# Kernel optimization log

Measured on AMD Instinct MI355X. Metric: run time of the kernel, lower is better.

Reference implementation:

```python
import jax, jax.numpy as jnp
import numpy as np
from jax import lax

# --- dims (match init_kwargs / mambapy defaults) ---
D_MODEL = 128
D_STATE = 64
D_CONV = 4
EXPAND = 2
ED = EXPAND * D_MODEL          # 256, d_inner
DT_RANK = (D_MODEL + 15) // 16 # 8, mambapy 'auto'
B_SZ, T = 4, 1024
EPS = 1e-5


def setup_inputs() -> dict:
    key = jax.random.key(0)
    ks = jax.random.split(key, 16)
    s = 0.02
    return {
        "z_seq": jax.random.normal(ks[0], (B_SZ, T, D_MODEL), jnp.float32),
        "aux_tensor": jax.random.normal(ks[1], (B_SZ, T, 3), jnp.float32),
        # wrapper params
        "aux_W": jax.random.normal(ks[2], (D_MODEL, 3), jnp.float32) * s,
        "aux_b": jnp.zeros((D_MODEL,), jnp.float32),
        "ln_w": jnp.ones((D_MODEL,), jnp.float32),
        "ln_b": jnp.zeros((D_MODEL,), jnp.float32),
        # mambapy ResidualBlock RMSNorm
        "rms_w": jnp.ones((D_MODEL,), jnp.float32),
        # MambaBlock params
        "in_proj_W": jax.random.normal(ks[3], (2 * ED, D_MODEL), jnp.float32) * s,
        "conv_W": jax.random.normal(ks[4], (ED, 1, D_CONV), jnp.float32) * s,  # depthwise (O,I/g,K)
        "conv_b": jnp.zeros((ED,), jnp.float32),
        "x_proj_W": jax.random.normal(ks[5], (DT_RANK + 2 * D_STATE, ED), jnp.float32) * s,
        "dt_W": jax.random.normal(ks[6], (ED, DT_RANK), jnp.float32) * s,
        "dt_b": jax.random.uniform(ks[7], (ED,), jnp.float32, -4.0, -2.0),  # softplus -> small dt
        "A_log": jnp.log(jnp.broadcast_to(jnp.arange(1, D_STATE + 1, dtype=jnp.float32), (ED, D_STATE))),
        "D_param": jnp.ones((ED,), jnp.float32),
        "out_proj_W": jax.random.normal(ks[8], (D_MODEL, ED), jnp.float32) * s,
    }


def _mamba_block(x, conv_W, conv_b, in_proj_W, x_proj_W, dt_W, dt_b, A_log, D_param, out_proj_W):
    # x: (B,T,D_MODEL) -> (B,T,D_MODEL)
    xz = x @ in_proj_W.T                             # (B,T,2*ED)
    xs, zg = xz[..., :ED], xz[..., ED:]
    # causal depthwise conv1d over time
    xc = lax.conv_general_dilated(
        xs.transpose(0, 2, 1), conv_W, (1,), ((D_CONV - 1, 0),),
        feature_group_count=ED, dimension_numbers=("NCH", "OIH", "NCH"))
    xs = jax.nn.silu((xc + conv_b[None, :, None]).transpose(0, 2, 1))  # (B,T,ED)
    dbc = xs @ x_proj_W.T                            # (B,T,DT_RANK+2N)
    delta = jax.nn.softplus(dbc[..., :DT_RANK] @ dt_W.T + dt_b)  # (B,T,ED)
    Bm = dbc[..., DT_RANK:DT_RANK + D_STATE]          # (B,T,N)
    Cm = dbc[..., DT_RANK + D_STATE:]                 # (B,T,N)
    A = -jnp.exp(A_log)                               # (ED,N)
    deltaA = jnp.exp(delta[..., None] * A)            # (B,T,ED,N)
    BX = (delta * xs)[..., None] * Bm[:, :, None, :]  # (B,T,ED,N)

    def combine(e1, e2):
        a1, b1 = e1
        a2, b2 = e2
        return a2 * a1, a2 * b1 + b2

    _, h = lax.associative_scan(combine, (deltaA, BX), axis=1)  # h: (B,T,ED,N)
    y = jnp.einsum("bten,btn->bte", h, Cm) + D_param * xs
    y = y * jax.nn.silu(zg)
    return y @ out_proj_W.T


def reference(z_seq, aux_tensor, aux_W, aux_b, ln_w, ln_b, rms_w,
              in_proj_W, conv_W, conv_b, x_proj_W, dt_W, dt_b, A_log, D_param, out_proj_W):
    # wrapper: aux injection
    z = z_seq + aux_tensor @ aux_W.T + aux_b         # (B,T,D)
    # mambapy ResidualBlock: mixer(RMSNorm(z)) + z
    zn = z * lax.rsqrt(jnp.mean(z * z, -1, keepdims=True) + EPS) * rms_w
    core = _mamba_block(zn, conv_W, conv_b, in_proj_W, x_proj_W, dt_W, dt_b,
                        A_log, D_param, out_proj_W) + z
    # wrapper LayerNorm(core + z)
    r = core + z
    mu = jnp.mean(r, -1, keepdims=True)
    var = jnp.mean((r - mu) ** 2, -1, keepdims=True)
    out = (r - mu) * lax.rsqrt(var + EPS) * ln_w + ln_b
    return out
```

## Files before the change

### kernel.cpp

```cpp
#include <hip/hip_runtime.h>
#include <hip/hip_bf16.h>

#define B_SZ 4
#define T_SEQ 1024
#define DM 128
#define ED_ 256
#define NS 64
#define LOG2E 1.44269504088896340736f

#define OFF_Z      0u
#define OFF_ZG     524288u
#define OFF_XSR    1572864u
#define OFF_WC     2621440u
#define OFF_YR     2719744u
#define OFF_DPX    3768320u
#define OFF_BC     5865472u

__device__ __forceinline__ float sigmoidf_(float x){ return 1.f/(1.f+__expf(-x)); }
__device__ __forceinline__ float exp2_(float x){ return __builtin_amdgcn_exp2f(x); }
__device__ __forceinline__ float rlane_(float v, int l){
  return __int_as_float(__builtin_amdgcn_readlane(__float_as_int(v), l));
}

#define DPPR(p, ctl) asm("v_add_f32_dpp %0, %0, %0 " ctl " row_mask:0xf bank_mask:0xf bound_ctrl:0" : "+v"(p))
#define DPP6(p) do{ DPPR(p,"row_shr:1"); DPPR(p,"row_shr:2"); DPPR(p,"row_shr:4"); \
                    DPPR(p,"row_shr:8"); DPPR(p,"row_bcast:15"); DPPR(p,"row_bcast:31"); }while(0)

__global__ __launch_bounds__(256) void k0_t(const float* W, float* WTi){
  int k4 = blockIdx.x >> 1;
  int c  = (blockIdx.x & 1)*256 + threadIdx.x;
  float4 w = *(const float4*)&W[(size_t)c*128 + 4*k4];
  ((float4*)WTi)[k4*512 + c] = w;
}

__global__ __launch_bounds__(256) void k2_fused(const float* zseq, const float* aux, const float* auxW,
                                                const float* auxb, const float* rmsw, const float* WTi,
                                                const float* xprojW, const float* dtW,
                                                float* z, float* xsr, float* zg, float* WcT){
  if (blockIdx.x >= 512){
    int r = blockIdx.x - 512; int k = threadIdx.x;
    float v;
    if (r < 256){
      v = 0.f;
      #pragma unroll
      for (int j=0;j<8;j++) v += dtW[r*8+j] * xprojW[j*256+k];
    } else {
      v = xprojW[(8 + r-256)*256 + k];
    }
    WcT[((k>>2)*384 + r)*4 + (k&3)] = v;
    return;
  }
  __shared__ float at[128][8];
  int bt0 = blockIdx.x*8; int tid = threadIdx.x;
  {
    int r = tid>>5, l = tid&31;
    int bt = bt0 + r;
    float a0 = aux[bt*3+0], a1 = aux[bt*3+1], a2 = aux[bt*3+2];
    float zv[4]; float ssq = 0.f;
    #pragma unroll
    for (int j=0;j<4;j++){
      int d = l + 32*j;
      float v = zseq[bt*DM+d] + a0*auxW[d*3+0] + a1*auxW[d*3+1] + a2*auxW[d*3+2] + auxb[d];
      zv[j] = v; ssq += v*v;
    }
    #pragma unroll
    for (int m=16;m>=1;m>>=1) ssq += __shfl_xor(ssq, m);
    float rinv = rsqrtf(ssq*(1.f/DM) + 1e-5f);
    #pragma unroll
    for (int j=0;j<4;j++){
      int d = l + 32*j;
      z[bt*DM+d] = zv[j];
      at[d][r] = zv[j]*rinv*rmsw[d];
    }
  }
  __syncthreads();
  float acc0[8], acc1[8];
  #pragma unroll
  for (int r=0;r<8;r++){ acc0[r]=0.f; acc1[r]=0.f; }
  int c0 = tid;
  const float4* WTv = (const float4*)WTi;
  for (int k4=0;k4<32;k4++){
    float4 w0 = WTv[k4*512 + c0];
    float4 w1 = WTv[k4*512 + c0 + 256];
    float w0a[4] = {w0.x,w0.y,w0.z,w0.w};
    float w1a[4] = {w1.x,w1.y,w1.z,w1.w};
    #pragma unroll
    for (int kk=0;kk<4;kk++){
      float a[8];
      *(float4*)&a[0] = *(const float4*)&at[4*k4+kk][0];
      *(float4*)&a[4] = *(const float4*)&at[4*k4+kk][4];
      #pragma unroll
      for (int r=0;r<8;r++){ acc0[r] = fmaf(a[r], w0a[kk], acc0[r]); acc1[r] = fmaf(a[r], w1a[kk], acc1[r]); }
    }
  }
  #pragma unroll
  for (int r=0;r<8;r++){
    int bt = bt0+r;
    xsr[bt*ED_ + c0] = acc0[r];
    zg [bt*ED_ + c0] = acc1[r];
  }
}

__global__ __launch_bounds__(384) void k4b_xproj(const float* xsr, const float* convW, const float* convb,
                                                 const float* WcT, const float* dtb,
                                                 float* dxp, float* bcf){
  __shared__ float at[256][8];
  int bt0 = blockIdx.x*8; int tid = threadIdx.x;
  for (int i=tid;i<2048;i+=384){
    int r=i>>8,k=i&255; int bt=bt0+r; int t = bt & (T_SEQ-1);
    float4 wv = *(const float4*)(convW + k*4);
    float s = convb[k];
    if (t>=3) s += xsr[(bt-3)*ED_+k]*wv.x;
    if (t>=2) s += xsr[(bt-2)*ED_+k]*wv.y;
    if (t>=1) s += xsr[(bt-1)*ED_+k]*wv.z;
    s += xsr[bt*ED_+k]*wv.w;
    at[k][r] = s * sigmoidf_(s);
  }
  __syncthreads();
  float acc[8];
  #pragma unroll
  for (int r=0;r<8;r++) acc[r]=0.f;
  int c = tid;
  const float4* Wv = (const float4*)WcT;
  for (int k4=0;k4<64;k4++){
    float4 w = Wv[k4*384 + c];
    float wa[4] = {w.x,w.y,w.z,w.w};
    #pragma unroll
    for (int kk=0;kk<4;kk++){
      float a[8];
      *(float4*)&a[0] = *(const float4*)&at[4*k4+kk][0];
      *(float4*)&a[4] = *(const float4*)&at[4*k4+kk][4];
      #pragma unroll
      for (int r=0;r<8;r++) acc[r] = fmaf(a[r], wa[kk], acc[r]);
    }
  }
  int b4 = bt0 >> 10, tb = bt0 & (T_SEQ-1);
  if (c < 256){
    float bcv = dtb[c];
    float2* pout = (float2*)dxp + (size_t)(b4*ED_ + c)*T_SEQ + tb;
    #pragma unroll
    for (int r=0;r<8;r++){
      float xv = acc[r] + bcv;
      float dv = (xv > 20.f) ? xv : log1pf(__expf(xv));
      pout[r] = make_float2(dv, dv * at[c][r]);
    }
  } else if (c < 320){
    #pragma unroll
    for (int r=0;r<8;r++) bcf[((size_t)(bt0+r)*NS + (c-256))*2 + 0] = acc[r];
  } else {
    #pragma unroll
    for (int r=0;r<8;r++) bcf[((size_t)(bt0+r)*NS + (c-320))*2 + 1] = acc[r];
  }
}

__global__ __launch_bounds__(512,4) void k5_scan(const float* dxpf, const float* bcf,
                                                  const float* Alog, float* yrT,
                                                  const float* outW, float* wot){
  if (blockIdx.x >= 512){
    int idx = (blockIdx.x - 512)*512 + threadIdx.x;
    int k4 = idx >> 7;
    int d  = idx & 127;
    float4 v = *(const float4*)&outW[(size_t)d*256 + 4*k4];
    ((float4*)wot)[k4*128 + d] = v;
    return;
  }
  __shared__ float lcar[7][2][64], lapr[7][2][64];
  __shared__ float red[8][16][2][66];
  int i  = blockIdx.x;
  int tid = threadIdx.x;
  int wv = tid >> 6;
  int n  = tid & 63;
  int x = i & 7;
  int r = i >> 3;
  int b = r & 3;
  int g = r >> 2;
  int eA = x*32 + g*2;
  int eB = eA + 1;
  const int CH = T_SEQ/8;
  int t0 = wv*CH;
  float A2A = -__expf(Alog[eA*NS+n]) * LOG2E;
  float A2B = -__expf(Alog[eB*NS+n]) * LOG2E;
  const float2* pdA = (const float2*)dxpf + (size_t)(b*ED_ + eA)*T_SEQ + t0;
  const float2* pdB = (const float2*)dxpf + (size_t)(b*ED_ + eB)*T_SEQ + t0;
  const float2* pbc = (const float2*)bcf  + (size_t)(b*T_SEQ + t0)*NS + n;
  float* pyA = yrT + (size_t)(b*ED_ + eA)*T_SEQ + t0;
  float* pyB = yrT + (size_t)(b*ED_ + eB)*T_SEQ + t0;

  if (wv < 7){
    float hA=0.f, hB=0.f, SsA=0.f, SsB=0.f;
    float2 dxcA = pdA[n], dxcB = pdB[n];
    for (int sb=0; sb<CH; sb+=64){
      float2 dxnA = dxcA, dxnB = dxcB;
      if (sb+64 < CH){ dxnA = pdA[sb+64+n]; dxnB = pdB[sb+64+n]; }
      float svA = dxcA.x; DPP6(svA); SsA += rlane_(svA, 63);
      float svB = dxcB.x; DPP6(svB); SsB += rlane_(svB, 63);
      float bA[8], bBv[8];
      #pragma unroll
      for (int j=0;j<8;j++) bA[j] = pbc[(sb+j)*NS].x;
      #pragma unroll
      for (int bb=0; bb<64; bb+=16){
        #pragma unroll
        for (int j=0;j<8;j++) bBv[j] = pbc[(sb+bb+8+j)*NS].x;
        #pragma unroll
        for (int j=0;j<8;j++){
          float sdA = rlane_(dxcA.x, bb+j), suA = rlane_(dxcA.y, bb+j);
          hA = fmaf(exp2_(sdA*A2A), hA, suA*bA[j]);
          float sdB = rlane_(dxcB.x, bb+j), suB = rlane_(dxcB.y, bb+j);
          hB = fmaf(exp2_(sdB*A2B), hB, suB*bA[j]);
        }
        if (bb+16 < 64){
          #pragma unroll
          for (int j=0;j<8;j++) bA[j] = pbc[(sb+bb+16+j)*NS].x;
        }
        #pragma unroll
        for (int j=0;j<8;j++){
          float sdA = rlane_(dxcA.x, bb+8+j), suA = rlane_(dxcA.y, bb+8+j);
          hA = fmaf(exp2_(sdA*A2A), hA, suA*bBv[j]);
          float sdB = rlane_(dxcB.x, bb+8+j), suB = rlane_(dxcB.y, bb+8+j);
          hB = fmaf(exp2_(sdB*A2B), hB, suB*bBv[j]);
        }
      }
      dxcA = dxnA; dxcB = dxnB;
    }
    lcar[wv][0][n] = hA;  lapr[wv][0][n] = exp2_(A2A*SsA);
    lcar[wv][1][n] = hB;  lapr[wv][1][n] = exp2_(A2B*SsB);
  }
  __syncthreads();

  float hA = 0.f, hB = 0.f;
  #pragma unroll
  for (int q=0;q<7;q++) if (wv > q){
    hA = fmaf(lapr[q][0][n], hA, lcar[q][0][n]);
    hB = fmaf(lapr[q][1][n], hB, lcar[q][1][n]);
  }

  {
    float2 dxcA = pdA[n], dxcB = pdB[n];
    int ri = n & 31, hs = n >> 5;
    int eh = ri >> 4, tr = ri & 15;
    const float2* rp = (const float2*)&red[wv][tr][eh][hs*32];
    float* pyE = eh ? pyB : pyA;
    for (int sb=0; sb<CH; sb+=64){
      float2 dxnA = dxcA, dxnB = dxcB;
      if (sb+64 < CH){ dxnA = pdA[sb+64+n]; dxnB = pdB[sb+64+n]; }
      float2 cA[8], cB[8];
      #pragma unroll
      for (int j=0;j<8;j++) cA[j] = pbc[(sb+j)*NS];
      #pragma unroll
      for (int bb=0; bb<64; bb+=16){
        #pragma unroll
        for (int j=0;j<8;j++) cB[j] = pbc[(sb+bb+8+j)*NS];
        #pragma unroll
        for (int j=0;j<8;j++){
          float sdA = rlane_(dxcA.x, bb+j), suA = rlane_(dxcA.y, bb+j);
          hA = fmaf(exp2_(sdA*A2A), hA, suA*cA[j].x);
          red[wv][j][0][n] = hA*cA[j].y;
          float sdB = rlane_(dxcB.x, bb+j), suB = rlane_(dxcB.y, bb+j);
          hB = fmaf(exp2_(sdB*A2B), hB, suB*cA[j].x);
          red[wv][j][1][n] = hB*cA[j].y;
        }
        if (bb+16 < 64){
          #pragma unroll
          for (int j=0;j<8;j++) cA[j] = pbc[(sb+bb+16+j)*NS];
        }
        #pragma unroll
        for (int j=0;j<8;j++){
          float sdA = rlane_(dxcA.x, bb+8+j), suA = rlane_(dxcA.y, bb+8+j);
          hA = fmaf(exp2_(sdA*A2A), hA, suA*cB[j].x);
          red[wv][8+j][0][n] = hA*cB[j].y;
          float sdB = rlane_(dxcB.x, bb+8+j), suB = rlane_(dxcB.y, bb+8+j);
          hB = fmaf(exp2_(sdB*A2B), hB, suB*cB[j].x);
          red[wv][8+j][1][n] = hB*cB[j].y;
        }
        float s = 0.f;
        #pragma unroll
        for (int jj=0;jj<16;jj++){ float2 v = rp[jj]; s += v.x + v.y; }
        s += __shfl_xor(s, 32);
        if (n < 32) pyE[sb + bb + tr] = s;
      }
      dxcA = dxnA; dxcB = dxnB;
    }
  }
}

__global__ __launch_bounds__(256) void k6_out(const float* yrT, const float* dxpf, const float* zg,
                                               const float* Dp, const float* wot, const float* z,
                                               const float* lnw, const float* lnb, float* out){
  __shared__ float yt[256][8];
  __shared__ float xst[256][8];
  __shared__ float psum[4][4], psq[4][4];
  int bt0 = blockIdx.x*8; int tid = threadIdx.x;
  int b4 = bt0 >> 10, tb = bt0 & (T_SEQ-1);
  int el = tid>>3, tl = tid&7;
  #pragma unroll
  for (int gg=0; gg<8; gg++){
    int ee = el + gg*32;
    size_t base = (size_t)(b4*ED_ + ee)*T_SEQ + tb + tl;
    float2 du = ((const float2*)dxpf)[base];
    yt[ee][tl]  = yrT[base];
    xst[ee][tl] = du.y / du.x;
  }
  __syncthreads();
  for (int i=tid;i<2048;i+=256){
    int rr=i>>8, k=i&255; int bt=bt0+rr;
    float zgv = zg[bt*ED_ + k];
    float yv  = yt[k][rr] + Dp[k]*xst[k][rr];
    yt[k][rr] = yv * zgv * sigmoidf_(zgv);
  }
  __syncthreads();
  int d = tid & 127, gdx = tid>>7;
  float acc[4] = {0.f,0.f,0.f,0.f};
  const float4* Wv = (const float4*)wot;
  for (int k4=0;k4<64;k4++){
    float4 w = Wv[k4*128 + d];
    int k = k4*4;
    float4 q0 = *(const float4*)&yt[k+0][gdx*4];
    float4 q1 = *(const float4*)&yt[k+1][gdx*4];
    float4 q2 = *(const float4*)&yt[k+2][gdx*4];
    float4 q3 = *(const float4*)&yt[k+3][gdx*4];
    acc[0] = fmaf(q0.x,w.x,acc[0]); acc[1] = fmaf(q0.y,w.x,acc[1]);
    acc[2] = fmaf(q0.z,w.x,acc[2]); acc[3] = fmaf(q0.w,w.x,acc[3]);
    acc[0] = fmaf(q1.x,w.y,acc[0]); acc[1] = fmaf(q1.y,w.y,acc[1]);
    acc[2] = fmaf(q1.z,w.y,acc[2]); acc[3] = fmaf(q1.w,w.y,acc[3]);
    acc[0] = fmaf(q2.x,w.z,acc[0]); acc[1] = fmaf(q2.y,w.z,acc[1]);
    acc[2] = fmaf(q2.z,w.z,acc[2]); acc[3] = fmaf(q2.w,w.z,acc[3]);
    acc[0] = fmaf(q3.x,w.w,acc[0]); acc[1] = fmaf(q3.y,w.w,acc[1]);
    acc[2] = fmaf(q3.z,w.w,acc[2]); acc[3] = fmaf(q3.w,w.w,acc[3]);
  }
  float val[4];
  #pragma unroll
  for (int j=0;j<4;j++){
    int bt = bt0 + gdx*4 + j;
    val[j] = acc[j] + 2.f*z[bt*DM + d];
  }
  int w_id = tid>>6;
  #pragma unroll
  for (int j=0;j<4;j++){
    float s = val[j], q = val[j]*val[j];
    #pragma unroll
    for (int off=32; off>=1; off>>=1){ s += __shfl_down(s, off); q += __shfl_down(q, off); }
    if ((tid&63)==0){ psum[w_id][j]=s; psq[w_id][j]=q; }
  }
  __syncthreads();
  float lw = lnw[d], lb = lnb[d];
  #pragma unroll
  for (int j=0;j<4;j++){
    int bt = bt0 + gdx*4 + j;
    float sum = psum[gdx*2][j] + psum[gdx*2+1][j];
    float sq  = psq [gdx*2][j] + psq [gdx*2+1][j];
    float mu  = sum*(1.f/DM);
    float var = sq*(1.f/DM) - mu*mu;
    float inv = rsqrtf(var + 1e-5f);
    out[bt*DM + d] = (val[j]-mu)*inv*lw + lb;
  }
}

extern "C" void kernel_launch(void* const* d_in, const int* in_sizes, int n_in,
                              void* d_out, int out_size, void* d_ws, size_t ws_size,
                              hipStream_t stream){
  const float* zseq = (const float*)d_in[0];
  const float* aux  = (const float*)d_in[1];
  const float* auxW = (const float*)d_in[2];
  const float* auxb = (const float*)d_in[3];
  const float* lnw  = (const float*)d_in[4];
  const float* lnb  = (const float*)d_in[5];
  const float* rmsw = (const float*)d_in[6];
  const float* inW  = (const float*)d_in[7];
  const float* convW= (const float*)d_in[8];
  const float* convb= (const float*)d_in[9];
  const float* xpW  = (const float*)d_in[10];
  const float* dtW  = (const float*)d_in[11];
  const float* dtb  = (const float*)d_in[12];
  const float* Alog = (const float*)d_in[13];
  const float* Dp   = (const float*)d_in[14];
  const float* outW = (const float*)d_in[15];
  float* out = (float*)d_out;
  float* ws = (float*)d_ws;

  float* z   = ws+OFF_Z;
  float* zg  = ws+OFF_ZG;
  float* xsr = ws+OFF_XSR;
  float* wot = ws+OFF_XSR;
  float* WcT = ws+OFF_WC;
  float* yr  = ws+OFF_YR;
  float* wti = ws+OFF_YR;
  float* dxp = ws+OFF_DPX;
  float* bcp = ws+OFF_BC;

  k0_t     <<<64,256,0,stream>>>(inW, wti);
  k2_fused <<<896,256,0,stream>>>(zseq,aux,auxW,auxb,rmsw,wti,xpW,dtW,z,xsr,zg,WcT);
  k4b_xproj<<<512,384,0,stream>>>(xsr,convW,convb,WcT,dtb,dxp,bcp);
  k5_scan  <<<528,512,0,stream>>>(dxp,bcp,Alog,yr,outW,wot);
  k6_out   <<<512,256,0,stream>>>(yr,dxp,zg,Dp,wot,z,lnw,lnb,out);
}
```

Measured before the change: 178.5 us.

## Process four channels per scan block to reuse B/C loads across channels

The chunked selective-scan kernel now handles four d_inner channels per block instead of two, which halves the number of scan blocks and the grid. Each B/C load from global memory is shared across twice as many channel recurrences, and the carry buffers are aliased onto the reduction shared array to free LDS. The trade-off is higher register pressure, serialised two-pass reductions through shared memory, fewer blocks to fill the GPU, and the loss of the next-chunk prefetch of dx.

After: 183.0 us. 1.03x slower.

```diff
diff --git a/kernel.cpp b/kernel.cpp
--- a/kernel.cpp
+++ b/kernel.cpp
@@ -156,16 +156,17 @@
 __global__ __launch_bounds__(512,4) void k5_scan(const float* dxpf, const float* bcf,
                                                   const float* Alog, float* yrT,
                                                   const float* outW, float* wot){
-  if (blockIdx.x >= 512){
-    int idx = (blockIdx.x - 512)*512 + threadIdx.x;
+  if (blockIdx.x >= 256){
+    int idx = (blockIdx.x - 256)*512 + threadIdx.x;
     int k4 = idx >> 7;
     int d  = idx & 127;
     float4 v = *(const float4*)&outW[(size_t)d*256 + 4*k4];
     ((float4*)wot)[k4*128 + d] = v;
     return;
   }
-  __shared__ float lcar[7][2][64], lapr[7][2][64];
   __shared__ float red[8][16][2][66];
+  float* lcarF = (float*)red;
+  float* laprF = lcarF + 7*4*64;
   int i  = blockIdx.x;
   int tid = threadIdx.x;
   int wv = tid >> 6;
@@ -173,40 +174,38 @@
   int x = i & 7;
   int r = i >> 3;
   int b = r & 3;
-  int g = r >> 2;
-  int eA = x*32 + g*2;
-  int eB = eA + 1;
+  int gg = r >> 2;
+  int e0 = x*32 + gg*4;
   const int CH = T_SEQ/8;
   int t0 = wv*CH;
-  float A2A = -__expf(Alog[eA*NS+n]) * LOG2E;
-  float A2B = -__expf(Alog[eB*NS+n]) * LOG2E;
-  const float2* pdA = (const float2*)dxpf + (size_t)(b*ED_ + eA)*T_SEQ + t0;
-  const float2* pdB = (const float2*)dxpf + (size_t)(b*ED_ + eB)*T_SEQ + t0;
-  const float2* pbc = (const float2*)bcf  + (size_t)(b*T_SEQ + t0)*NS + n;
-  float* pyA = yrT + (size_t)(b*ED_ + eA)*T_SEQ + t0;
-  float* pyB = yrT + (size_t)(b*ED_ + eB)*T_SEQ + t0;
+  float A2[4];
+  #pragma unroll
+  for (int e=0;e<4;e++) A2[e] = -__expf(Alog[(e0+e)*NS+n]) * LOG2E;
+  const float2* pbc = (const float2*)bcf + (size_t)(b*T_SEQ + t0)*NS + n;
+  const float2* pd0 = (const float2*)dxpf + (size_t)(b*ED_ + e0)*T_SEQ + t0;
 
   if (wv < 7){
-    float hA=0.f, hB=0.f, SsA=0.f, SsB=0.f;
-    float2 dxcA = pdA[n], dxcB = pdB[n];
+    float h[4] = {0.f,0.f,0.f,0.f}, Ss[4] = {0.f,0.f,0.f,0.f};
     for (int sb=0; sb<CH; sb+=64){
-      float2 dxnA = dxcA, dxnB = dxcB;
-      if (sb+64 < CH){ dxnA = pdA[sb+64+n]; dxnB = pdB[sb+64+n]; }
-      float svA = dxcA.x; DPP6(svA); SsA += rlane_(svA, 63);
-      float svB = dxcB.x; DPP6(svB); SsB += rlane_(svB, 63);
-      float bA[8], bBv[8];
+      float2 dxc[4];
+      #pragma unroll
+      for (int e=0;e<4;e++) dxc[e] = pd0[(size_t)e*T_SEQ + sb + n];
+      #pragma unroll
+      for (int e=0;e<4;e++){ float sv = dxc[e].x; DPP6(sv); Ss[e] += rlane_(sv, 63); }
+      float bA[8], bB[8];
       #pragma unroll
       for (int j=0;j<8;j++) bA[j] = pbc[(sb+j)*NS].x;
       #pragma unroll
       for (int bb=0; bb<64; bb+=16){
         #pragma unroll
-        for (int j=0;j<8;j++) bBv[j] = pbc[(sb+bb+8+j)*NS].x;
+        for (int j=0;j<8;j++) bB[j] = pbc[(sb+bb+8+j)*NS].x;
         #pragma unroll
         for (int j=0;j<8;j++){
-          float sdA = rlane_(dxcA.x, bb+j), suA = rlane_(dxcA.y, bb+j);
-          hA = fmaf(exp2_(sdA*A2A), hA, suA*bA[j]);
-          float sdB = rlane_(dxcB.x, bb+j), suB = rlane_(dxcB.y, bb+j);
-          hB = fmaf(exp2_(sdB*A2B), hB, suB*bA[j]);
+          #pragma unroll
+          for (int e=0;e<4;e++){
+            float sd = rlane_(dxc[e].x, bb+j), su = rlane_(dxc[e].y, bb+j);
+            h[e] = fmaf(exp2_(sd*A2[e]), h[e], su*bA[j]);
+          }
         }
         if (bb+16 < 64){
           #pragma unroll
@@ -214,71 +213,98 @@
         }
         #pragma unroll
         for (int j=0;j<8;j++){
-          float sdA = rlane_(dxcA.x, bb+8+j), suA = rlane_(dxcA.y, bb+8+j);
-          hA = fmaf(exp2_(sdA*A2A), hA, suA*bBv[j]);
-          float sdB = rlane_(dxcB.x, bb+8+j), suB = rlane_(dxcB.y, bb+8+j);
-          hB = fmaf(exp2_(sdB*A2B), hB, suB*bBv[j]);
+          #pragma unroll
+          for (int e=0;e<4;e++){
+            float sd = rlane_(dxc[e].x, bb+8+j), su = rlane_(dxc[e].y, bb+8+j);
+            h[e] = fmaf(exp2_(sd*A2[e]), h[e], su*bB[j]);
+          }
         }
       }
-      dxcA = dxnA; dxcB = dxnB;
-    }
-    lcar[wv][0][n] = hA;  lapr[wv][0][n] = exp2_(A2A*SsA);
-    lcar[wv][1][n] = hB;  lapr[wv][1][n] = exp2_(A2B*SsB);
-  }
-  __syncthreads();
-
-  float hA = 0.f, hB = 0.f;
+    }
+    #pragma unroll
+    for (int e=0;e<4;e++){
+      lcarF[(wv*4+e)*64+n] = h[e];
+      laprF[(wv*4+e)*64+n] = exp2_(A2[e]*Ss[e]);
+    }
+  }
+  __syncthreads();
+
+  float h[4] = {0.f,0.f,0.f,0.f};
   #pragma unroll
   for (int q=0;q<7;q++) if (wv > q){
-    hA = fmaf(lapr[q][0][n], hA, lcar[q][0][n]);
-    hB = fmaf(lapr[q][1][n], hB, lcar[q][1][n]);
-  }
+    #pragma unroll
+    for (int e=0;e<4;e++)
+      h[e] = fmaf(laprF[(q*4+e)*64+n], h[e], lcarF[(q*4+e)*64+n]);
+  }
+  __syncthreads();
 
   {
-    float2 dxcA = pdA[n], dxcB = pdB[n];
     int ri = n & 31, hs = n >> 5;
     int eh = ri >> 4, tr = ri & 15;
     const float2* rp = (const float2*)&red[wv][tr][eh][hs*32];
-    float* pyE = eh ? pyB : pyA;
+    float* py0e = yrT + (size_t)(b*ED_ + e0 + eh    )*T_SEQ + t0;
+    float* py1e = yrT + (size_t)(b*ED_ + e0 + 2 + eh)*T_SEQ + t0;
     for (int sb=0; sb<CH; sb+=64){
-      float2 dxnA = dxcA, dxnB = dxcB;
-      if (sb+64 < CH){ dxnA = pdA[sb+64+n]; dxnB = pdB[sb+64+n]; }
-      float2 cA[8], cB[8];
-      #pragma unroll
-      for (int j=0;j<8;j++) cA[j] = pbc[(sb+j)*NS];
-      #pragma unroll
+      float2 dxc[4];
+      #pragma unroll
+      for (int e=0;e<4;e++) dxc[e] = pd0[(size_t)e*T_SEQ + sb + n];
       for (int bb=0; bb<64; bb+=16){
-        #pragma unroll
-        for (int j=0;j<8;j++) cB[j] = pbc[(sb+bb+8+j)*NS];
+        float pp2[16], pp3[16];
+        float2 cA[8];
+        #pragma unroll
+        for (int j=0;j<8;j++) cA[j] = pbc[(sb+bb+j)*NS];
         #pragma unroll
         for (int j=0;j<8;j++){
-          float sdA = rlane_(dxcA.x, bb+j), suA = rlane_(dxcA.y, bb+j);
-          hA = fmaf(exp2_(sdA*A2A), hA, suA*cA[j].x);
-          red[wv][j][0][n] = hA*cA[j].y;
-          float sdB = rlane_(dxcB.x, bb+j), suB = rlane_(dxcB.y, bb+j);
-          hB = fmaf(exp2_(sdB*A2B), hB, suB*cA[j].x);
-          red[wv][j][1][n] = hB*cA[j].y;
-        }
-        if (bb+16 < 64){
+          float sd0 = rlane_(dxc[0].x, bb+j), su0 = rlane_(dxc[0].y, bb+j);
+          h[0] = fmaf(exp2_(sd0*A2[0]), h[0], su0*cA[j].x);
+          red[wv][j][0][n] = h[0]*cA[j].y;
+          float sd1 = rlane_(dxc[1].x, bb+j), su1 = rlane_(dxc[1].y, bb+j);
+          h[1] = fmaf(exp2_(sd1*A2[1]), h[1], su1*cA[j].x);
+          red[wv][j][1][n] = h[1]*cA[j].y;
+          float sd2 = rlane_(dxc[2].x, bb+j), su2 = rlane_(dxc[2].y, bb+j);
+          h[2] = fmaf(exp2_(sd2*A2[2]), h[2], su2*cA[j].x);
+          pp2[j] = h[2]*cA[j].y;
+          float sd3 = rlane_(dxc[3].x, bb+j), su3 = rlane_(dxc[3].y, bb+j);
+          h[3] = fmaf(exp2_(sd3*A2[3]), h[3], su3*cA[j].x);
+          pp3[j] = h[3]*cA[j].y;
+        }
+        #pragma unroll
+        for (int j=0;j<8;j++) cA[j] = pbc[(sb+bb+8+j)*NS];
+        #pragma unroll
+        for (int j=0;j<8;j++){
+          float sd0 = rlane_(dxc[0].x, bb+8+j), su0 = rlane_(dxc[0].y, bb+8+j);
+          h[0] = fmaf(exp2_(sd0*A2[0]), h[0], su0*cA[j].x);
+          red[wv][8+j][0][n] = h[0]*cA[j].y;
+          float sd1 = rlane_(dxc[1].x, bb+8+j), su1 = rlane_(dxc[1].y, bb+8+j);
+          h[1] = fmaf(exp2_(sd1*A2[1]), h[1], su1*cA[j].x);
+          red[wv][8+j][1][n] = h[1]*cA[j].y;
+          float sd2 = rlane_(dxc[2].x, bb+8+j), su2 = rlane_(dxc[2].y, bb+8+j);
+          h[2] = fmaf(exp2_(sd2*A2[2]), h[2], su2*cA[j].x);
+          pp2[8+j] = h[2]*cA[j].y;
+          float sd3 = rlane_(dxc[3].x, bb+8+j), su3 = rlane_(dxc[3].y, bb+8+j);
+          h[3] = fmaf(exp2_(sd3*A2[3]), h[3], su3*cA[j].x);
+          pp3[8+j] = h[3]*cA[j].y;
+        }
+        {
+          float s = 0.f;
           #pragma unroll
-          for (int j=0;j<8;j++) cA[j] = pbc[(sb+bb+16+j)*NS];
-        }
-        #pragma unroll
-        for (int j=0;j<8;j++){
-          float sdA = rlane_(dxcA.x, bb+8+j), suA = rlane_(dxcA.y, bb+8+j);
-          hA = fmaf(exp2_(sdA*A2A), hA, suA*cB[j].x);
-          red[wv][8+j][0][n] = hA*cB[j].y;
-          float sdB = rlane_(dxcB.x, bb+8+j), suB = rlane_(dxcB.y, bb+8+j);
-          hB = fmaf(exp2_(sdB*A2B), hB, suB*cB[j].x);
-          red[wv][8+j][1][n] = hB*cB[j].y;
-        }
-        float s = 0.f;
-        #pragma unroll
-        for (int jj=0;jj<16;jj++){ float2 v = rp[jj]; s += v.x + v.y; }
-        s += __shfl_xor(s, 32);
-        if (n < 32) pyE[sb + bb + tr] = s;
+          for (int jj=0;jj<16;jj++){ float2 v = rp[jj]; s += v.x + v.y; }
+          s += __shfl_xor(s, 32);
+          if (n < 32) py0e[sb + bb + tr] = s;
+        }
+        #pragma unroll
+        for (int j=0;j<16;j++){
+          red[wv][j][0][n] = pp2[j];
+          red[wv][j][1][n] = pp3[j];
+        }
+        {
+          float s = 0.f;
+          #pragma unroll
+          for (int jj=0;jj<16;jj++){ float2 v = rp[jj]; s += v.x + v.y; }
+          s += __shfl_xor(s, 32);
+          if (n < 32) py1e[sb + bb + tr] = s;
+        }
       }
-      dxcA = dxnA; dxcB = dxnB;
     }
   }
 }
@@ -390,6 +416,6 @@
   k0_t     <<<64,256,0,stream>>>(inW, wti);
   k2_fused <<<896,256,0,stream>>>(zseq,aux,auxW,auxb,rmsw,wti,xpW,dtW,z,xsr,zg,WcT);
   k4b_xproj<<<512,384,0,stream>>>(xsr,convW,convb,WcT,dtb,dxp,bcp);
-  k5_scan  <<<528,512,0,stream>>>(dxp,bcp,Alog,yr,outW,wot);
+  k5_scan  <<<272,512,0,stream>>>(dxp,bcp,Alog,yr,outW,wot);
   k6_out   <<<512,256,0,stream>>>(yr,dxp,zg,Dp,wot,z,lnw,lnb,out);
 }
```

## Widen GEMM kernels with split-K thread halves to raise parallelism

Applied to the files above, without the earlier changes.

Three GEMM-style kernels (in_proj, x_proj, out_proj) now launch more threads per block. In k2, each thread computes one output column instead of two. In k4b and k6, the K dimension is split across two thread halves whose partial sums are combined through shared memory. The goal is more waves in flight to hide latency on the small fp32 GEMMs, which otherwise run with few active waves. The cost is extra shared memory, an added barrier, and idle threads during the epilogue and the WcT-build blocks.

New measurement: 174.5 us. 1.02x faster.

```diff
diff --git a/kernel.cpp b/kernel.cpp
--- a/kernel.cpp
+++ b/kernel.cpp
@@ -33,11 +33,12 @@
   ((float4*)WTi)[k4*512 + c] = w;
 }
 
-__global__ __launch_bounds__(256) void k2_fused(const float* zseq, const float* aux, const float* auxW,
+__global__ __launch_bounds__(512,4) void k2_fused(const float* zseq, const float* aux, const float* auxW,
                                                 const float* auxb, const float* rmsw, const float* WTi,
                                                 const float* xprojW, const float* dtW,
                                                 float* z, float* xsr, float* zg, float* WcT){
   if (blockIdx.x >= 512){
+    if (threadIdx.x >= 256) return;
     int r = blockIdx.x - 512; int k = threadIdx.x;
     float v;
     if (r < 256){
@@ -53,60 +54,61 @@
   __shared__ float at[128][8];
   int bt0 = blockIdx.x*8; int tid = threadIdx.x;
   {
-    int r = tid>>5, l = tid&31;
+    int r = tid>>6, l = tid&63;
     int bt = bt0 + r;
     float a0 = aux[bt*3+0], a1 = aux[bt*3+1], a2 = aux[bt*3+2];
-    float zv[4]; float ssq = 0.f;
-    #pragma unroll
-    for (int j=0;j<4;j++){
-      int d = l + 32*j;
+    float zv[2]; float ssq = 0.f;
+    #pragma unroll
+    for (int j=0;j<2;j++){
+      int d = l + 64*j;
       float v = zseq[bt*DM+d] + a0*auxW[d*3+0] + a1*auxW[d*3+1] + a2*auxW[d*3+2] + auxb[d];
       zv[j] = v; ssq += v*v;
     }
     #pragma unroll
-    for (int m=16;m>=1;m>>=1) ssq += __shfl_xor(ssq, m);
+    for (int m=32;m>=1;m>>=1) ssq += __shfl_xor(ssq, m);
     float rinv = rsqrtf(ssq*(1.f/DM) + 1e-5f);
     #pragma unroll
-    for (int j=0;j<4;j++){
-      int d = l + 32*j;
+    for (int j=0;j<2;j++){
+      int d = l + 64*j;
       z[bt*DM+d] = zv[j];
       at[d][r] = zv[j]*rinv*rmsw[d];
     }
   }
   __syncthreads();
-  float acc0[8], acc1[8];
+  float acc[8];
   #pragma unroll
-  for (int r=0;r<8;r++){ acc0[r]=0.f; acc1[r]=0.f; }
+  for (int r=0;r<8;r++) acc[r]=0.f;
   int c0 = tid;
   const float4* WTv = (const float4*)WTi;
   for (int k4=0;k4<32;k4++){
-    float4 w0 = WTv[k4*512 + c0];
-    float4 w1 = WTv[k4*512 + c0 + 256];
-    float w0a[4] = {w0.x,w0.y,w0.z,w0.w};
-    float w1a[4] = {w1.x,w1.y,w1.z,w1.w};
+    float4 w = WTv[k4*512 + c0];
+    float wa[4] = {w.x,w.y,w.z,w.w};
     #pragma unroll
     for (int kk=0;kk<4;kk++){
       float a[8];
       *(float4*)&a[0] = *(const float4*)&at[4*k4+kk][0];
       *(float4*)&a[4] = *(const float4*)&at[4*k4+kk][4];
       #pragma unroll
-      for (int r=0;r<8;r++){ acc0[r] = fmaf(a[r], w0a[kk], acc0[r]); acc1[r] = fmaf(a[r], w1a[kk], acc1[r]); }
-    }
-  }
-  #pragma unroll
-  for (int r=0;r<8;r++){
-    int bt = bt0+r;
-    xsr[bt*ED_ + c0] = acc0[r];
-    zg [bt*ED_ + c0] = acc1[r];
-  }
-}
-
-__global__ __launch_bounds__(384) void k4b_xproj(const float* xsr, const float* convW, const float* convb,
+      for (int r=0;r<8;r++) acc[r] = fmaf(a[r], wa[kk], acc[r]);
+    }
+  }
+  if (c0 < 256){
+    #pragma unroll
+    for (int r=0;r<8;r++) xsr[(bt0+r)*ED_ + c0] = acc[r];
+  } else {
+    int c1 = c0 - 256;
+    #pragma unroll
+    for (int r=0;r<8;r++) zg[(bt0+r)*ED_ + c1] = acc[r];
+  }
+}
+
+__global__ __launch_bounds__(768,6) void k4b_xproj(const float* xsr, const float* convW, const float* convb,
                                                  const float* WcT, const float* dtb,
                                                  float* dxp, float* bcf){
   __shared__ float at[256][8];
+  __shared__ float pacc[384][8];
   int bt0 = blockIdx.x*8; int tid = threadIdx.x;
-  for (int i=tid;i<2048;i+=384){
+  for (int i=tid;i<2048;i+=768){
     int r=i>>8,k=i&255; int bt=bt0+r; int t = bt & (T_SEQ-1);
     float4 wv = *(const float4*)(convW + k*4);
     float s = convb[k];
@@ -120,9 +122,12 @@
   float acc[8];
   #pragma unroll
   for (int r=0;r<8;r++) acc[r]=0.f;
-  int c = tid;
+  int half = (tid >= 384);
+  int c = half ? (tid - 384) : tid;
   const float4* Wv = (const float4*)WcT;
-  for (int k4=0;k4<64;k4++){
+  int k40 = half ? 32 : 0;
+  for (int kq=0;kq<32;kq++){
+    int k4 = k40 + kq;
     float4 w = Wv[k4*384 + c];
     float wa[4] = {w.x,w.y,w.z,w.w};
     #pragma unroll
@@ -134,22 +139,31 @@
       for (int r=0;r<8;r++) acc[r] = fmaf(a[r], wa[kk], acc[r]);
     }
   }
-  int b4 = bt0 >> 10, tb = bt0 & (T_SEQ-1);
-  if (c < 256){
-    float bcv = dtb[c];
-    float2* pout = (float2*)dxp + (size_t)(b4*ED_ + c)*T_SEQ + tb;
-    #pragma unroll
-    for (int r=0;r<8;r++){
-      float xv = acc[r] + bcv;
-      float dv = (xv > 20.f) ? xv : log1pf(__expf(xv));
-      pout[r] = make_float2(dv, dv * at[c][r]);
-    }
-  } else if (c < 320){
-    #pragma unroll
-    for (int r=0;r<8;r++) bcf[((size_t)(bt0+r)*NS + (c-256))*2 + 0] = acc[r];
-  } else {
-    #pragma unroll
-    for (int r=0;r<8;r++) bcf[((size_t)(bt0+r)*NS + (c-320))*2 + 1] = acc[r];
+  if (half){
+    #pragma unroll
+    for (int r=0;r<8;r++) pacc[c][r] = acc[r];
+  }
+  __syncthreads();
+  if (!half){
+    #pragma unroll
+    for (int r=0;r<8;r++) acc[r] += pacc[c][r];
+    int b4 = bt0 >> 10, tb = bt0 & (T_SEQ-1);
+    if (c < 256){
+      float bcv = dtb[c];
+      float2* pout = (float2*)dxp + (size_t)(b4*ED_ + c)*T_SEQ + tb;
+      #pragma unroll
+      for (int r=0;r<8;r++){
+        float xv = acc[r] + bcv;
+        float dv = (xv > 20.f) ? xv : log1pf(__expf(xv));
+        pout[r] = make_float2(dv, dv * at[c][r]);
+      }
+    } else if (c < 320){
+      #pragma unroll
+      for (int r=0;r<8;r++) bcf[((size_t)(bt0+r)*NS + (c-256))*2 + 0] = acc[r];
+    } else {
+      #pragma unroll
+      for (int r=0;r<8;r++) bcf[((size_t)(bt0+r)*NS + (c-320))*2 + 1] = acc[r];
+    }
   }
 }
 
@@ -283,35 +297,40 @@
   }
 }
 
-__global__ __launch_bounds__(256) void k6_out(const float* yrT, const float* dxpf, const float* zg,
+__global__ __launch_bounds__(512,4) void k6_out(const float* yrT, const float* dxpf, const float* zg,
                                                const float* Dp, const float* wot, const float* z,
                                                const float* lnw, const float* lnb, float* out){
   __shared__ float yt[256][8];
   __shared__ float xst[256][8];
+  __shared__ float pacc[256][4];
   __shared__ float psum[4][4], psq[4][4];
   int bt0 = blockIdx.x*8; int tid = threadIdx.x;
   int b4 = bt0 >> 10, tb = bt0 & (T_SEQ-1);
   int el = tid>>3, tl = tid&7;
   #pragma unroll
-  for (int gg=0; gg<8; gg++){
-    int ee = el + gg*32;
+  for (int gg=0; gg<4; gg++){
+    int ee = el + gg*64;
     size_t base = (size_t)(b4*ED_ + ee)*T_SEQ + tb + tl;
     float2 du = ((const float2*)dxpf)[base];
     yt[ee][tl]  = yrT[base];
     xst[ee][tl] = du.y / du.x;
   }
   __syncthreads();
-  for (int i=tid;i<2048;i+=256){
+  for (int i=tid;i<2048;i+=512){
     int rr=i>>8, k=i&255; int bt=bt0+rr;
     float zgv = zg[bt*ED_ + k];
     float yv  = yt[k][rr] + Dp[k]*xst[k][rr];
     yt[k][rr] = yv * zgv * sigmoidf_(zgv);
   }
   __syncthreads();
-  int d = tid & 127, gdx = tid>>7;
+  int d = tid & 127;
+  int quad = tid >> 7;
+  int gdx = quad & 1, half = quad >> 1;
   float acc[4] = {0.f,0.f,0.f,0.f};
   const float4* Wv = (const float4*)wot;
-  for (int k4=0;k4<64;k4++){
+  int k40 = half ? 32 : 0;
+  for (int kq=0;kq<32;kq++){
+    int k4 = k40 + kq;
     float4 w = Wv[k4*128 + d];
     int k = k4*4;
     float4 q0 = *(const float4*)&yt[k+0][gdx*4];
@@ -327,31 +346,42 @@
     acc[0] = fmaf(q3.x,w.w,acc[0]); acc[1] = fmaf(q3.y,w.w,acc[1]);
     acc[2] = fmaf(q3.z,w.w,acc[2]); acc[3] = fmaf(q3.w,w.w,acc[3]);
   }
+  if (half){
+    #pragma unroll
+    for (int j=0;j<4;j++) pacc[gdx*128+d][j] = acc[j];
+  }
+  __syncthreads();
   float val[4];
-  #pragma unroll
-  for (int j=0;j<4;j++){
-    int bt = bt0 + gdx*4 + j;
-    val[j] = acc[j] + 2.f*z[bt*DM + d];
-  }
-  int w_id = tid>>6;
-  #pragma unroll
-  for (int j=0;j<4;j++){
-    float s = val[j], q = val[j]*val[j];
-    #pragma unroll
-    for (int off=32; off>=1; off>>=1){ s += __shfl_down(s, off); q += __shfl_down(q, off); }
-    if ((tid&63)==0){ psum[w_id][j]=s; psq[w_id][j]=q; }
-  }
-  __syncthreads();
-  float lw = lnw[d], lb = lnb[d];
-  #pragma unroll
-  for (int j=0;j<4;j++){
-    int bt = bt0 + gdx*4 + j;
-    float sum = psum[gdx*2][j] + psum[gdx*2+1][j];
-    float sq  = psq [gdx*2][j] + psq [gdx*2+1][j];
-    float mu  = sum*(1.f/DM);
-    float var = sq*(1.f/DM) - mu*mu;
-    float inv = rsqrtf(var + 1e-5f);
-    out[bt*DM + d] = (val[j]-mu)*inv*lw + lb;
+  if (!half){
+    #pragma unroll
+    for (int j=0;j<4;j++) acc[j] += pacc[gdx*128+d][j];
+    #pragma unroll
+    for (int j=0;j<4;j++){
+      int bt = bt0 + gdx*4 + j;
+      val[j] = acc[j] + 2.f*z[bt*DM + d];
+    }
+    int w_id = tid>>6;
+    #pragma unroll
+    for (int j=0;j<4;j++){
+      float s = val[j], q = val[j]*val[j];
+      #pragma unroll
+      for (int off=32; off>=1; off>>=1){ s += __shfl_down(s, off); q += __shfl_down(q, off); }
+      if ((tid&63)==0){ psum[w_id][j]=s; psq[w_id][j]=q; }
+    }
+  }
+  __syncthreads();
+  if (!half){
+    float lw = lnw[d], lb = lnb[d];
+    #pragma unroll
+    for (int j=0;j<4;j++){
+      int bt = bt0 + gdx*4 + j;
+      float sum = psum[gdx*2][j] + psum[gdx*2+1][j];
+      float sq  = psq [gdx*2][j] + psq [gdx*2+1][j];
+      float mu  = sum*(1.f/DM);
+      float var = sq*(1.f/DM) - mu*mu;
+      float inv = rsqrtf(var + 1e-5f);
+      out[bt*DM + d] = (val[j]-mu)*inv*lw + lb;
+    }
   }
 }
 
@@ -388,8 +418,8 @@
   float* bcp = ws+OFF_BC;
 
   k0_t     <<<64,256,0,stream>>>(inW, wti);
-  k2_fused <<<896,256,0,stream>>>(zseq,aux,auxW,auxb,rmsw,wti,xpW,dtW,z,xsr,zg,WcT);
-  k4b_xproj<<<512,384,0,stream>>>(xsr,convW,convb,WcT,dtb,dxp,bcp);
+  k2_fused <<<896,512,0,stream>>>(zseq,aux,auxW,auxb,rmsw,wti,xpW,dtW,z,xsr,zg,WcT);
+  k4b_xproj<<<512,768,0,stream>>>(xsr,convW,convb,WcT,dtb,dxp,bcp);
   k5_scan  <<<528,512,0,stream>>>(dxp,bcp,Alog,yr,outW,wot);
-  k6_out   <<<512,256,0,stream>>>(yr,dxp,zg,Dp,wot,z,lnw,lnb,out);
-}
+  k6_out   <<<512,512,0,stream>>>(yr,dxp,zg,Dp,wot,z,lnw,lnb,out);
+}
```
